# Performance work log

Measured on AMD Instinct MI355X. Metric: run time of the kernel, lower is better.

## Reference

```python
import math
import jax, jax.numpy as jnp
import numpy as np

D_MODEL = 768
N_HEAD = 12
N_BR = 4
DH = D_MODEL // N_HEAD          # 64
H_TOT = N_BR * N_HEAD           # 48
SCALE = math.pi / math.sqrt(3.0)
ATTNSCALE = DH ** -0.5


def _chebyshev(T, max_deg, dtype):
    # T_all[t, d] = Cheb poly T_d(x_t), x in [-1, 1]
    if T > 1:
        x = 2.0 * jnp.arange(T, dtype=dtype) / (T - 1) - 1.0
    else:
        x = jnp.zeros(1, dtype=dtype)
    cols = [jnp.ones_like(x), x]
    for _ in range(2, max_deg + 1):
        cols.append(2.0 * x * cols[-1] - cols[-2])
    return jnp.stack(cols, axis=1)  # (T, max_deg+1)


def setup_inputs() -> dict:
    key = jax.random.key(0)
    ks = jax.random.split(key, 12)
    s = 0.02
    return {
        "X": jax.random.normal(ks[0], (2, 1024, D_MODEL), jnp.float32),
        "Wq": jax.random.normal(ks[1], (D_MODEL * N_BR, D_MODEL), jnp.float32) * s,
        "bq": jax.random.normal(ks[2], (D_MODEL * N_BR,), jnp.float32) * s,
        "Wk": jax.random.normal(ks[3], (D_MODEL, D_MODEL), jnp.float32) * s,
        "bk": jax.random.normal(ks[4], (D_MODEL,), jnp.float32) * s,
        "Wv": jax.random.normal(ks[5], (D_MODEL, D_MODEL), jnp.float32) * s,
        "bv": jax.random.normal(ks[6], (D_MODEL,), jnp.float32) * s,
        "A": jax.random.normal(ks[7], (DH, DH), jnp.float32) * s,
        "id_bias": jax.random.normal(ks[8], (H_TOT, DH), jnp.float32) * s,
        "sink_scalars": jax.random.normal(ks[9], (H_TOT, 1, 1), jnp.float32) * s,
        "v_nulls": jax.random.normal(ks[10], (N_BR, D_MODEL), jnp.float32) * s,
        "Wo": jax.random.normal(ks[11], (N_BR, D_MODEL, D_MODEL), jnp.float32) * s,
        "bo": jnp.zeros((N_BR, D_MODEL), jnp.float32),
    }


def _attention(X, Wq, bq, Wk, bk, Wv, bv, A, id_bias, sink_scalars, v_nulls, Wo, bo):
    B, T, C = X.shape
    dtype = X.dtype

    # projections (torch Linear: x @ W.T + b)
    q = (X @ Wq.T + bq).reshape(B, T, H_TOT, DH).transpose(0, 2, 1, 3)   # (B,H_tot,T,Dh)
    v = (X @ Wv.T + bv).reshape(B, T, N_HEAD, DH).transpose(0, 2, 1, 3)
    v = jnp.tile(v, (1, N_BR, 1, 1))                                     # (B,H_tot,T,Dh)
    k = (X @ Wk.T + bk).reshape(B, T, N_HEAD, DH).transpose(0, 2, 1, 3)
    k = jnp.tile(k, (1, N_BR, 1, 1))

    # BiasedWedge on q
    S = (A - A.T)[None] + jax.vmap(jnp.diag)(id_bias)                    # (H_tot,Dh,Dh)
    q = q + jnp.einsum('bhtd,hde->bhte', q, S)

    # Chebyshev phase-vector rotation (custom RoPE)
    H = DH // 2
    max_deg = max(3, 2 * H)
    T_all = _chebyshev(T, max_deg, dtype)                                # (T, max_deg+1)
    frac = jnp.arange(H, dtype=dtype) / (H - 1) if H > 1 else jnp.zeros(1, dtype)
    n_f = jnp.clip(1 + jnp.round(frac * (max_deg - 2)).astype(jnp.int32), 1, max_deg - 1)
    raw1 = T_all[:, n_f]                                                 # (T,H)
    raw2 = T_all[:, n_f + 1]
    nrm = jnp.sqrt(raw1 * raw1 + raw2 * raw2 + 1e-8)
    base1 = (raw1 / nrm)[None, None]                                     # (1,1,T,H)
    base2 = (raw2 / nrm)[None, None]

    def apply_rot(x_in):
        x1, x2 = x_in[..., :H], x_in[..., H:]
        return jnp.concatenate([x1 * base1 - x2 * base2,
                                x1 * base2 + x2 * base1], axis=-1)

    q = apply_rot(q)
    k = apply_rot(k)

    # softplus-gated causal attention with learned sink
    scores = jnp.einsum('bhtd,bhsd->bhts', q, k) * ATTNSCALE             # (B,H_tot,T,T)
    key_self = jnp.maximum((k * k).sum(-1), 1e-6)                        # (B,H_tot,T)
    denom = jnp.sqrt(key_self)[:, :, None, :]
    w = jax.nn.softplus(scores / denom)
    causal = jnp.tril(jnp.ones((T, T), bool))                            # keep lower-tri
    w = jnp.where(causal, w, 0.0)
    w = w * jax.nn.sigmoid(SCALE * w)

    sinks = sink_scalars.reshape(1, H_TOT, 1, 1)                         # broadcast sink col
    alpha = 1.0 / (w.sum(-1, keepdims=True) + sinks + 1e-6)              # (B,H_tot,T,1)
    probs_tokens = w * alpha
    probs_sink = jnp.broadcast_to(sinks, (B, H_TOT, T, 1)) * alpha

    out_tokens = jnp.einsum('bhts,bhsd->bhtd', probs_tokens, v)
    v_null = v_nulls.reshape(H_TOT, DH)[None, :, None, :]                # (1,H_tot,1,Dh)
    context = out_tokens + probs_sink * v_null                           # (B,H_tot,T,Dh)

    context = context.reshape(B, N_BR, N_HEAD, T, DH)
    context = context.transpose(0, 1, 3, 2, 4).reshape(B, N_BR, T, C)
    y = jnp.einsum('bntc,ncd->bntd', context, Wo) + bo[None, :, None, :]
    return y.mean(axis=1)                                                # (B,T,C)


def reference(X, Wq, bq, Wk, bk, Wv, bv, A, id_bias, sink_scalars, v_nulls, Wo, bo):
    return _attention(X, Wq, bq, Wk, bk, Wv, bv, A, id_bias, sink_scalars, v_nulls, Wo, bo)
```

## Files before the change

kernel.cpp:

```cpp
#include <hip/hip_runtime.h>
#include <math.h>

#define B_ 2
#define T_ 1024
#define C_ 768
#define NH 12
#define NBR 4
#define DH_ 64
#define HT 48
#define MROWS (B_*T_)

#define SCALE_W 1.8137993642342178f
#define ATTNSCALE_ 0.125f

#define OFF_B1    0
#define OFF_B2    (OFF_B1 + 32768)
#define OFF_QKVB  (OFF_B2 + 32768)
#define OFF_BSUM  (OFF_QKVB + 4608)
#define OFF_WQKV  (OFF_BSUM + 768)
#define OFF_XB    (OFF_WQKV + 1769472)
#define OFF_WOT   (OFF_XB + 786432)
#define OFF_QF    (OFF_WOT + 1179648)
#define OFF_KF    (OFF_QF + 6291456)
#define OFF_VF    (OFF_KF + 1572864)
#define OFF_QB    OFF_KF
#define OFF_KB    (OFF_VF + 1572864)
#define OFF_VB    (OFF_KB + 786432)
#define OFF_RKS   (OFF_VB + 786432)
#define OFF_CTXB  OFF_QF

typedef __attribute__((ext_vector_type(8))) short short8t;
typedef __attribute__((ext_vector_type(4))) float f32x4;

__device__ inline ushort f2bf(float f) {
    union { float f; unsigned u; } v; v.f = f;
    unsigned r = (v.u + 0x7FFFu + ((v.u >> 16) & 1u)) >> 16;
    return (ushort)r;
}

typedef __attribute__((address_space(3))) void lds_vt;
typedef const __attribute__((address_space(1))) void gbl_vt;
static __device__ __forceinline__ void gload16(const void* g, void* l) {
    __builtin_amdgcn_global_load_lds((gbl_vt*)g, (lds_vt*)l, 16, 0, 0);
}

__global__ void cheb_kernel(float* __restrict__ ws) {
    int t = blockIdx.x * 256 + threadIdx.x;
    if (t >= T_) return;
    float* b1 = ws + OFF_B1 + t * 32;
    float* b2 = ws + OFF_B2 + t * 32;
    float x = 2.0f * (float)t / 1023.0f - 1.0f;
    float Tp = 1.0f, Tc = x;
    for (int j = 0; j < 32; j++) {
        float r1 = Tc;
        float r2 = 2.0f * x * Tc - Tp;
        float nr = sqrtf(r1 * r1 + r2 * r2 + 1e-8f);
        b1[j] = r1 / nr;
        b2[j] = r2 / nr;
        Tp = r2;
        Tc = 2.0f * x * r2 - r1;
    }
}

__global__ __launch_bounds__(256) void prep_wq(
    const float* __restrict__ Aw, const float* __restrict__ idb,
    const float* __restrict__ Wq, const float* __restrict__ bq,
    float* __restrict__ ws) {
    __shared__ float Ms[64][64];
    int h = blockIdx.x;
    int tid = threadIdx.x;
    for (int i = tid; i < 4096; i += 256) {
        int d = i >> 6, e = i & 63;
        float v = Aw[d * 64 + e] - Aw[e * 64 + d];
        if (d == e) v += 1.0f + idb[h * 64 + d];
        Ms[d][e] = v;
    }
    __syncthreads();
    int c = blockIdx.y * 256 + tid;
    float wq[64];
#pragma unroll
    for (int d = 0; d < 64; d++) wq[d] = Wq[(size_t)(h * 64 + d) * 768 + c];
    ushort* EWqb = (ushort*)(ws + OFF_WQKV);
    for (int e = 0; e < 64; e++) {
        float acc = 0.f;
#pragma unroll
        for (int d = 0; d < 64; d++) acc += Ms[d][e] * wq[d];
        EWqb[(size_t)(h * 64 + e) * 768 + c] = f2bf(acc);
    }
    if (blockIdx.y == 0 && tid < 64) {
        int e = tid;
        float acc = 0.f;
        for (int d = 0; d < 64; d++) acc += Ms[d][e] * bq[h * 64 + d];
        ws[OFF_QKVB + h * 64 + e] = acc;
    }
}

__global__ void conv_bf16(const float* __restrict__ src, ushort* __restrict__ dst) {
    int i = (blockIdx.x * 256 + threadIdx.x) * 4;
    float4 v = *(const float4*)(src + i);
    ushort4 o;
    o.x = f2bf(v.x); o.y = f2bf(v.y); o.z = f2bf(v.z); o.w = f2bf(v.w);
    *(ushort4*)(dst + i) = o;
}

__global__ __launch_bounds__(256) void woT_kernel(const float* __restrict__ Wo,
                                                  ushort* __restrict__ WoT) {
    __shared__ float tile[64][65];
    int nb = blockIdx.z;
    int k0 = blockIdx.x * 64, c0 = blockIdx.y * 64;
    int tx = threadIdx.x & 63, ty = threadIdx.x >> 6;
#pragma unroll
    for (int p = 0; p < 16; p++) {
        int ky = p * 4 + ty;
        tile[ky][tx] = Wo[((size_t)nb * 768 + k0 + ky) * 768 + c0 + tx];
    }
    __syncthreads();
#pragma unroll
    for (int p = 0; p < 16; p++) {
        int cy = p * 4 + ty;
        WoT[(size_t)(c0 + cy) * 3072 + nb * 768 + k0 + tx] = f2bf(tile[tx][cy]);
    }
}

__global__ void bias_prep(const float* __restrict__ bo, const float* __restrict__ bk,
                          const float* __restrict__ bv, float* __restrict__ ws) {
    int n = blockIdx.x * 256 + threadIdx.x;
    if (n < 768) {
        ws[OFF_BSUM + n] = 0.25f * (bo[n] + bo[768 + n] + bo[1536 + n] + bo[2304 + n]);
        ws[OFF_QKVB + 3072 + n] = bk[n];
        ws[OFF_QKVB + 3840 + n] = bv[n];
    }
}

__global__ void y_init(const float* __restrict__ bsum, float* __restrict__ Y) {
    int idx = (blockIdx.x * 256 + threadIdx.x) * 4;
    int n = idx - (idx / 768) * 768;
    float4 o = { bsum[n], bsum[n + 1], bsum[n + 2], bsum[n + 3] };
    *(float4*)(Y + idx) = o;
}

static __device__ __forceinline__ void gemm_kloop128(
    const ushort* __restrict__ A, const ushort* __restrict__ B, int K,
    int m0, int n0, int k_begin, int k_end,
    ushort* AsU, ushort* BsU, f32x4 acc[4][4], int tid) {
    char* As = (char*)AsU;
    char* Bs = (char*)BsU;
    int lane = tid & 63, w = tid >> 6;
    int g = lane >> 4, c = lane & 15;
    int wr = w >> 1, wc = w & 1;
    int srow[4], scol[4];
#pragma unroll
    for (int r = 0; r < 4; r++) {
        int p = r * 4096 + w * 1024 + lane * 16;
        int row = p >> 7;
        int bp = (p & 127) ^ ((row & 7) << 4);
        srow[r] = row;
        scol[r] = bp >> 1;
    }
    for (int k0 = k_begin; k0 < k_end; k0 += 64) {
        __syncthreads();
#pragma unroll
        for (int r = 0; r < 4; r++) {
            gload16(A + (size_t)(m0 + srow[r]) * K + k0 + scol[r],
                    As + r * 4096 + w * 1024);
            gload16(B + (size_t)(n0 + srow[r]) * K + k0 + scol[r],
                    Bs + r * 4096 + w * 1024);
        }
        __syncthreads();
#pragma unroll
        for (int kk = 0; kk < 2; kk++) {
            short8t af[4], bf[4];
#pragma unroll
            for (int i = 0; i < 4; i++) {
                int ra = wr * 64 + i * 16 + c;
                af[i] = *(const short8t*)(As + ra * 128 + ((kk * 64 + g * 16) ^ ((ra & 7) << 4)));
                int rb = wc * 64 + i * 16 + c;
                bf[i] = *(const short8t*)(Bs + rb * 128 + ((kk * 64 + g * 16) ^ ((rb & 7) << 4)));
            }
#pragma unroll
            for (int i = 0; i < 4; i++)
#pragma unroll
                for (int j = 0; j < 4; j++)
                    acc[i][j] = __builtin_amdgcn_mfma_f32_16x16x32_bf16(
                        af[i], bf[j], acc[i][j], 0, 0, 0);
        }
    }
}

__global__ __launch_bounds__(256) void gemm_qkv(
    const ushort* __restrict__ A, const ushort* __restrict__ Bw,
    const float* __restrict__ qkvbias,
    float* __restrict__ Q, float* __restrict__ Kf, float* __restrict__ Vf) {
    __shared__ __align__(16) ushort AsU[8192];
    __shared__ __align__(16) ushort BsU[8192];
    int tid = threadIdx.x;
    int lane = tid & 63, wid = tid >> 6;
    int wr = wid >> 1, wc = wid & 1;
    int g = lane >> 4, c = lane & 15;
    int m0 = blockIdx.x * 128, n0 = blockIdx.y * 128;
    f32x4 acc[4][4] = {};
    gemm_kloop128(A, Bw, 768, m0, n0, 0, 768, AsU, BsU, acc, tid);
    int y = blockIdx.y;
    float* outp; int nstr, nbase;
    if (y < 24)      { outp = Q;  nstr = 3072; nbase = 0; }
    else if (y < 30) { outp = Kf; nstr = 768;  nbase = 3072; }
    else             { outp = Vf; nstr = 768;  nbase = 3840; }
#pragma unroll
    for (int j = 0; j < 4; j++) {
        int n = n0 + wc * 64 + j * 16 + c;
        float bv = qkvbias[n];
#pragma unroll
        for (int i = 0; i < 4; i++) {
#pragma unroll
            for (int r = 0; r < 4; r++) {
                int m = m0 + wr * 64 + i * 16 + g * 4 + r;
                outp[(size_t)m * nstr + (n - nbase)] = acc[i][j][r] + bv;
            }
        }
    }
}

__global__ __launch_bounds__(256) void gemm_fin(
    const ushort* __restrict__ A, const ushort* __restrict__ Bw,
    float* __restrict__ Y) {
    __shared__ __align__(16) ushort AsU[8192];
    __shared__ __align__(16) ushort BsU[8192];
    int tid = threadIdx.x;
    int lane = tid & 63, wid = tid >> 6;
    int wr = wid >> 1, wc = wid & 1;
    int g = lane >> 4, c = lane & 15;
    int m0 = blockIdx.x * 128, n0 = blockIdx.y * 128;
    int kz = blockIdx.z * 1024;
    f32x4 acc[4][4] = {};
    gemm_kloop128(A, Bw, 3072, m0, n0, kz, kz + 1024, AsU, BsU, acc, tid);
#pragma unroll
    for (int j = 0; j < 4; j++) {
        int n = n0 + wc * 64 + j * 16 + c;
#pragma unroll
        for (int i = 0; i < 4; i++) {
#pragma unroll
            for (int r = 0; r < 4; r++) {
                int m = m0 + wr * 64 + i * 16 + g * 4 + r;
                atomicAdd(&Y[(size_t)m * 768 + n], 0.25f * acc[i][j][r]);
            }
        }
    }
}

__global__ void rot2_kernel(const float* __restrict__ in, int heads,
                            ushort* __restrict__ outb, float* __restrict__ rkso,
                            const float* __restrict__ ws) {
    int idx = blockIdx.x * 256 + threadIdx.x;
    if (idx >= MROWS * heads) return;
    int r = idx / heads;
    int hd = idx - r * heads;
    int tloc = r & (T_ - 1);
    int b = r >> 10;
    const float* p = in + (size_t)r * (heads * 64) + hd * 64;
    const float* b1 = ws + OFF_B1 + tloc * 32;
    const float* b2 = ws + OFF_B2 + tloc * 32;
    __align__(16) ushort ob[64];
    float nrm = 0.f;
#pragma unroll
    for (int i = 0; i < 8; i++) {
        float4 lo = *(const float4*)(p + i * 4);
        float4 hi = *(const float4*)(p + 32 + i * 4);
        float4 c1 = *(const float4*)(b1 + i * 4);
        float4 c2 = *(const float4*)(b2 + i * 4);
        float o1[4], o2[4];
        o1[0] = lo.x * c1.x - hi.x * c2.x;  o2[0] = lo.x * c2.x + hi.x * c1.x;
        o1[1] = lo.y * c1.y - hi.y * c2.y;  o2[1] = lo.y * c2.y + hi.y * c1.y;
        o1[2] = lo.z * c1.z - hi.z * c2.z;  o2[2] = lo.z * c2.z + hi.z * c1.z;
        o1[3] = lo.w * c1.w - hi.w * c2.w;  o2[3] = lo.w * c2.w + hi.w * c1.w;
#pragma unroll
        for (int j = 0; j < 4; j++) {
            ob[i * 4 + j]      = f2bf(o1[j]);
            ob[32 + i * 4 + j] = f2bf(o2[j]);
            nrm += o1[j] * o1[j] + o2[j] * o2[j];
        }
    }
    ushort* op = outb + ((size_t)(b * heads + hd) * T_ + tloc) * 64;
#pragma unroll
    for (int i = 0; i < 8; i++) *(int4*)(op + i * 8) = *(const int4*)&ob[i * 8];
    if (rkso) rkso[((b * heads + hd) << 10) + tloc] = ATTNSCALE_ / sqrtf(fmaxf(nrm, 1e-6f));
}

__global__ void vconv_kernel(const float* __restrict__ V, ushort* __restrict__ Vb) {
    int idx = blockIdx.x * 256 + threadIdx.x;
    int base = idx * 4;
    int row = base / 768, col = base - row * 768;
    int b = row >> 10, t = row & (T_ - 1);
    int hk = col >> 6, d = col & 63;
    float4 v = *(const float4*)(V + (size_t)row * 768 + col);
    ushort4 o;
    o.x = f2bf(v.x); o.y = f2bf(v.y); o.z = f2bf(v.z); o.w = f2bf(v.w);
    *(ushort4*)(Vb + ((size_t)((b * NH + hk) * T_ + t)) * 64 + d) = o;
}

__global__ __launch_bounds__(512) void attn_mfma2(
    const ushort* __restrict__ Qb, const ushort* __restrict__ Kb,
    const ushort* __restrict__ Vb, const float* __restrict__ rks,
    const float* __restrict__ sinks, const float* __restrict__ vnull,
    ushort* __restrict__ ctxb) {
    __shared__ __align__(16) ushort Ks[64][72];
    __shared__ __align__(16) ushort Vt[64][72];
    __shared__ __align__(16) ushort Ps[8][16][72];
    __shared__ float rk_s[64];
    int tid  = threadIdx.x;
    int lane = tid & 63;
    int wid  = tid >> 6;
    int p = 7 - blockIdx.x;
    int bh = blockIdx.y;
    int b = bh / HT, h = bh - b * HT;
    int hk = h % NH;
    int qt0 = p * 128;
    int g = lane >> 4;
    int c = lane & 15;
    int rowbase = qt0 + wid * 16;

    const ushort* qrow = Qb + ((size_t)(b * HT + h) * T_ + rowbase + c) * 64;
    short8t qa0 = *(const short8t*)(qrow + g * 8);
    short8t qa1 = *(const short8t*)(qrow + 32 + g * 8);

    f32x4 oacc[4] = {};
    float sumw[4] = {0.f, 0.f, 0.f, 0.f};

    const size_t kvbase = (size_t)(b * NH + hk) * T_;
    int nt = 2 * p + 2;
    int sr = tid >> 3;
    int sc = (tid & 7) * 8;
    for (int st = 0; st < nt; st++) {
        int s0 = st * 64;
        __syncthreads();
        {
            *(int4*)&Ks[sr][sc] = *(const int4*)(Kb + (kvbase + s0 + sr) * 64 + sc);
            __align__(16) ushort vv[8];
            *(int4*)&vv[0] = *(const int4*)(Vb + (kvbase + s0 + sr) * 64 + sc);
#pragma unroll
            for (int j = 0; j < 8; j++) Vt[sc + j][sr] = vv[j];
            if (tid < 64) rk_s[tid] = rks[kvbase + (size_t)s0 + tid];
        }
        __syncthreads();

        if (s0 > rowbase + 15) continue;

        f32x4 sfr[4];
#pragma unroll
        for (int f = 0; f < 4; f++) {
            f32x4 cacc = {0.f, 0.f, 0.f, 0.f};
            short8t kb0 = *(const short8t*)&Ks[f * 16 + c][g * 8];
            cacc = __builtin_amdgcn_mfma_f32_16x16x32_bf16(qa0, kb0, cacc, 0, 0, 0);
            short8t kb1 = *(const short8t*)&Ks[f * 16 + c][32 + g * 8];
            cacc = __builtin_amdgcn_mfma_f32_16x16x32_bf16(qa1, kb1, cacc, 0, 0, 0);
            sfr[f] = cacc;
        }

        bool diag = (s0 + 63 > rowbase);
#pragma unroll
        for (int f = 0; f < 4; f++) {
            int scol = f * 16 + c;
            float rkv = rk_s[scol];
#pragma unroll
            for (int r = 0; r < 4; r++) {
                int trow = g * 4 + r;
                float x = sfr[f][r] * rkv;
                float w = __logf(1.f + __expf(x));
                w = w * __builtin_amdgcn_rcpf(1.f + __expf(-SCALE_W * w));
                if (diag && s0 + scol > rowbase + trow) w = 0.f;
                sumw[r] += w;
                Ps[wid][trow][scol] = f2bf(w);
            }
        }

#pragma unroll
        for (int hf = 0; hf < 2; hf++) {
            short8t pa = *(const short8t*)&Ps[wid][c][hf * 32 + g * 8];
#pragma unroll
            for (int f = 0; f < 4; f++) {
                short8t vb = *(const short8t*)&Vt[f * 16 + c][hf * 32 + g * 8];
                oacc[f] = __builtin_amdgcn_mfma_f32_16x16x32_bf16(pa, vb, oacc[f], 0, 0, 0);
            }
        }
    }

#pragma unroll
    for (int m = 1; m < 16; m <<= 1) {
#pragma unroll
        for (int r = 0; r < 4; r++) sumw[r] += __shfl_xor(sumw[r], m, 64);
    }
    float skv = sinks[h];
    float alpha[4], ps[4];
#pragma unroll
    for (int r = 0; r < 4; r++) {
        alpha[r] = 1.0f / (sumw[r] + skv + 1e-6f);
        ps[r] = skv * alpha[r];
    }
    int nb = h / NH;
#pragma unroll
    for (int f = 0; f < 4; f++) {
        float vn = vnull[h * 64 + f * 16 + c];
#pragma unroll
        for (int r = 0; r < 4; r++) {
            int t = rowbase + g * 4 + r;
            ctxb[(size_t)(b * T_ + t) * 3072 + nb * 768 + hk * 64 + f * 16 + c]
                = f2bf(oacc[f][r] * alpha[r] + ps[r] * vn);
        }
    }
}

extern "C" void kernel_launch(void* const* d_in, const int* in_sizes, int n_in,
                              void* d_out, int out_size, void* d_ws, size_t ws_size,
                              hipStream_t stream) {
    const float* X   = (const float*)d_in[0];
    const float* Wq  = (const float*)d_in[1];
    const float* bq  = (const float*)d_in[2];
    const float* Wk  = (const float*)d_in[3];
    const float* bk  = (const float*)d_in[4];
    const float* Wv  = (const float*)d_in[5];
    const float* bv  = (const float*)d_in[6];
    const float* Aw  = (const float*)d_in[7];
    const float* idb = (const float*)d_in[8];
    const float* sk  = (const float*)d_in[9];
    const float* vn  = (const float*)d_in[10];
    const float* Wo  = (const float*)d_in[11];
    const float* bo  = (const float*)d_in[12];
    float* ws = (float*)d_ws;
    float* Y  = (float*)d_out;

    ushort* WQKV = (ushort*)(ws + OFF_WQKV);
    hipLaunchKernelGGL(cheb_kernel, dim3(4), dim3(256), 0, stream, ws);
    hipLaunchKernelGGL(prep_wq, dim3(48, 3), dim3(256), 0, stream, Aw, idb, Wq, bq, ws);
    hipLaunchKernelGGL(conv_bf16, dim3(576), dim3(256), 0, stream,
                       Wk, WQKV + (size_t)3072 * 768);
    hipLaunchKernelGGL(conv_bf16, dim3(576), dim3(256), 0, stream,
                       Wv, WQKV + (size_t)3840 * 768);
    hipLaunchKernelGGL(conv_bf16, dim3(1536), dim3(256), 0, stream,
                       X, (ushort*)(ws + OFF_XB));
    hipLaunchKernelGGL(woT_kernel, dim3(12, 12, 4), dim3(256), 0, stream,
                       Wo, (ushort*)(ws + OFF_WOT));
    hipLaunchKernelGGL(bias_prep, dim3(3), dim3(256), 0, stream, bo, bk, bv, ws);
    hipLaunchKernelGGL(gemm_qkv, dim3(16, 36), dim3(256), 0, stream,
                       (const ushort*)(ws + OFF_XB), WQKV, ws + OFF_QKVB,
                       ws + OFF_QF, ws + OFF_KF, ws + OFF_VF);
    hipLaunchKernelGGL(rot2_kernel, dim3(96), dim3(256), 0, stream,
                       ws + OFF_KF, NH, (ushort*)(ws + OFF_KB), ws + OFF_RKS, ws);
    hipLaunchKernelGGL(vconv_kernel, dim3(1536), dim3(256), 0, stream,
                       ws + OFF_VF, (ushort*)(ws + OFF_VB));
    hipLaunchKernelGGL(rot2_kernel, dim3(384), dim3(256), 0, stream,
                       ws + OFF_QF, HT, (ushort*)(ws + OFF_QB), (float*)nullptr, ws);
    hipLaunchKernelGGL(attn_mfma2, dim3(8, 96), dim3(512), 0, stream,
                       (const ushort*)(ws + OFF_QB), (const ushort*)(ws + OFF_KB),
                       (const ushort*)(ws + OFF_VB), ws + OFF_RKS, sk, vn,
                       (ushort*)(ws + OFF_CTXB));
    hipLaunchKernelGGL(y_init, dim3(1536), dim3(256), 0, stream, ws + OFF_BSUM, Y);
    hipLaunchKernelGGL(gemm_fin, dim3(16, 6, 3), dim3(256), 0, stream,
                       (const ushort*)(ws + OFF_CTXB), (const ushort*)(ws + OFF_WOT), Y);
}
```

Baseline: 328.4 us.

## Share K/V tiles across four branch heads and pre-transpose V with swizzled LDS

The attention kernel now runs one block per (batch, KV head) and loops over the four branch query heads inside, so each K/V tile is loaded into shared memory once instead of four times. V is transposed to a d-major bf16 layout by a new LDS-tiled conversion kernel, which removes the per-element scatter transpose in the attention loop. K and V tiles are loaded with direct global-to-LDS loads (gload16) into XOR-swizzled layouts to avoid bank conflicts. The grid shrinks from 768 to 192 blocks and each thread holds four times the accumulators, which raises register pressure and may hurt occupancy and load balance.

Measured after the change: 363.8 us. +10.8%, slower.

```diff
diff --git a/kernel.cpp b/kernel.cpp
--- a/kernel.cpp
+++ b/kernel.cpp
@@ -285,125 +285,149 @@
     if (rkso) rkso[((b * heads + hd) << 10) + tloc] = ATTNSCALE_ / sqrtf(fmaxf(nrm, 1e-6f));
 }
 
-__global__ void vconv_kernel(const float* __restrict__ V, ushort* __restrict__ Vb) {
-    int idx = blockIdx.x * 256 + threadIdx.x;
-    int base = idx * 4;
-    int row = base / 768, col = base - row * 768;
-    int b = row >> 10, t = row & (T_ - 1);
-    int hk = col >> 6, d = col & 63;
-    float4 v = *(const float4*)(V + (size_t)row * 768 + col);
-    ushort4 o;
-    o.x = f2bf(v.x); o.y = f2bf(v.y); o.z = f2bf(v.z); o.w = f2bf(v.w);
-    *(ushort4*)(Vb + ((size_t)((b * NH + hk) * T_ + t)) * 64 + d) = o;
-}
-
-__global__ __launch_bounds__(512) void attn_mfma2(
+__global__ __launch_bounds__(256) void vconvT_kernel(const float* __restrict__ V,
+                                                     ushort* __restrict__ VbT) {
+    __shared__ float tile[64][65];
+    int head = blockIdx.y;
+    int b = head / NH, hk = head - b * NH;
+    int t0 = blockIdx.x * 64;
+    int tx = threadIdx.x & 63, ty = threadIdx.x >> 6;
+#pragma unroll
+    for (int p = 0; p < 16; p++) {
+        int trow = p * 4 + ty;
+        tile[trow][tx] = V[(size_t)(b * T_ + t0 + trow) * 768 + hk * 64 + tx];
+    }
+    __syncthreads();
+#pragma unroll
+    for (int p = 0; p < 16; p++) {
+        int d = p * 4 + ty;
+        VbT[(size_t)head * 65536 + (size_t)d * 1024 + t0 + tx] = f2bf(tile[tx][d]);
+    }
+}
+
+__global__ __launch_bounds__(512) void attn_mfma3(
     const ushort* __restrict__ Qb, const ushort* __restrict__ Kb,
-    const ushort* __restrict__ Vb, const float* __restrict__ rks,
+    const ushort* __restrict__ VbT, const float* __restrict__ rks,
     const float* __restrict__ sinks, const float* __restrict__ vnull,
     ushort* __restrict__ ctxb) {
-    __shared__ __align__(16) ushort Ks[64][72];
-    __shared__ __align__(16) ushort Vt[64][72];
-    __shared__ __align__(16) ushort Ps[8][16][72];
+    __shared__ __align__(16) char KsB[8192];
+    __shared__ __align__(16) char VtB[8192];
+    __shared__ __align__(16) char PsB[8][2048];
     __shared__ float rk_s[64];
     int tid  = threadIdx.x;
     int lane = tid & 63;
     int wid  = tid >> 6;
-    int p = 7 - blockIdx.x;
+    int p  = 7 - blockIdx.x;
     int bh = blockIdx.y;
-    int b = bh / HT, h = bh - b * HT;
-    int hk = h % NH;
+    int b = bh / NH, hk = bh - b * NH;
     int qt0 = p * 128;
     int g = lane >> 4;
     int c = lane & 15;
     int rowbase = qt0 + wid * 16;
 
-    const ushort* qrow = Qb + ((size_t)(b * HT + h) * T_ + rowbase + c) * 64;
-    short8t qa0 = *(const short8t*)(qrow + g * 8);
-    short8t qa1 = *(const short8t*)(qrow + 32 + g * 8);
-
-    f32x4 oacc[4] = {};
-    float sumw[4] = {0.f, 0.f, 0.f, 0.f};
+    short8t qa0[4], qa1[4];
+#pragma unroll
+    for (int nb = 0; nb < 4; nb++) {
+        const ushort* qrow = Qb +
+            ((size_t)(b * HT + nb * NH + hk) * T_ + rowbase + c) * 64;
+        qa0[nb] = *(const short8t*)(qrow + g * 8);
+        qa1[nb] = *(const short8t*)(qrow + 32 + g * 8);
+    }
+
+    f32x4 oacc[4][4] = {};
+    float sumw[4][4] = {};
 
     const size_t kvbase = (size_t)(b * NH + hk) * T_;
+    const ushort* Kt0 = Kb + kvbase * 64;
+    const ushort* Vt0 = VbT + kvbase * 64;
+    int drow  = tid >> 3;
+    int sbyte = ((tid & 7) * 16) ^ ((drow & 7) << 4);
+    int scolu = sbyte >> 1;
+    char* ldsK = KsB + wid * 1024;
+    char* ldsV = VtB + wid * 1024;
+
     int nt = 2 * p + 2;
-    int sr = tid >> 3;
-    int sc = (tid & 7) * 8;
     for (int st = 0; st < nt; st++) {
         int s0 = st * 64;
         __syncthreads();
-        {
-            *(int4*)&Ks[sr][sc] = *(const int4*)(Kb + (kvbase + s0 + sr) * 64 + sc);
-            __align__(16) ushort vv[8];
-            *(int4*)&vv[0] = *(const int4*)(Vb + (kvbase + s0 + sr) * 64 + sc);
-#pragma unroll
-            for (int j = 0; j < 8; j++) Vt[sc + j][sr] = vv[j];
-            if (tid < 64) rk_s[tid] = rks[kvbase + (size_t)s0 + tid];
-        }
+        gload16(Kt0 + (size_t)(s0 + drow) * 64 + scolu, ldsK);
+        gload16(Vt0 + (size_t)drow * 1024 + s0 + scolu, ldsV);
+        if (tid < 64) rk_s[tid] = rks[kvbase + (size_t)s0 + tid];
         __syncthreads();
 
         if (s0 > rowbase + 15) continue;
-
-        f32x4 sfr[4];
+        bool diag = (s0 + 63 > rowbase);
+        char* Ps = PsB[wid];
+
+#pragma unroll
+        for (int nb = 0; nb < 4; nb++) {
+            f32x4 sfr[4];
+#pragma unroll
+            for (int f = 0; f < 4; f++) {
+                int row = f * 16 + c, sw = (row & 7) << 4;
+                f32x4 cacc = {0.f, 0.f, 0.f, 0.f};
+                short8t kb0 = *(const short8t*)(KsB + row * 128 + ((g * 16) ^ sw));
+                cacc = __builtin_amdgcn_mfma_f32_16x16x32_bf16(qa0[nb], kb0, cacc, 0, 0, 0);
+                short8t kb1 = *(const short8t*)(KsB + row * 128 + ((64 + g * 16) ^ sw));
+                cacc = __builtin_amdgcn_mfma_f32_16x16x32_bf16(qa1[nb], kb1, cacc, 0, 0, 0);
+                sfr[f] = cacc;
+            }
+#pragma unroll
+            for (int f = 0; f < 4; f++) {
+                int scol = f * 16 + c;
+                float rkv = rk_s[scol];
+#pragma unroll
+                for (int r = 0; r < 4; r++) {
+                    int trow = g * 4 + r;
+                    float x = sfr[f][r] * rkv;
+                    float w = __logf(1.f + __expf(x));
+                    w = w * __builtin_amdgcn_rcpf(1.f + __expf(-SCALE_W * w));
+                    if (diag && s0 + scol > rowbase + trow) w = 0.f;
+                    sumw[nb][r] += w;
+                    *(ushort*)(Ps + trow * 128 + ((scol * 2) ^ ((trow & 7) << 4))) = f2bf(w);
+                }
+            }
+#pragma unroll
+            for (int hf = 0; hf < 2; hf++) {
+                short8t pa = *(const short8t*)(Ps + c * 128 +
+                                               ((hf * 64 + g * 16) ^ ((c & 7) << 4)));
+#pragma unroll
+                for (int f = 0; f < 4; f++) {
+                    int row = f * 16 + c;
+                    short8t vb = *(const short8t*)(VtB + row * 128 +
+                                                   ((hf * 64 + g * 16) ^ ((row & 7) << 4)));
+                    oacc[nb][f] = __builtin_amdgcn_mfma_f32_16x16x32_bf16(
+                        pa, vb, oacc[nb][f], 0, 0, 0);
+                }
+            }
+        }
+    }
+
+#pragma unroll
+    for (int nb = 0; nb < 4; nb++) {
+#pragma unroll
+        for (int m = 1; m < 16; m <<= 1) {
+#pragma unroll
+            for (int r = 0; r < 4; r++)
+                sumw[nb][r] += __shfl_xor(sumw[nb][r], m, 64);
+        }
+        int h = nb * NH + hk;
+        float skv = sinks[h];
+        float alpha[4], ps[4];
+#pragma unroll
+        for (int r = 0; r < 4; r++) {
+            alpha[r] = 1.0f / (sumw[nb][r] + skv + 1e-6f);
+            ps[r] = skv * alpha[r];
+        }
 #pragma unroll
         for (int f = 0; f < 4; f++) {
-            f32x4 cacc = {0.f, 0.f, 0.f, 0.f};
-            short8t kb0 = *(const short8t*)&Ks[f * 16 + c][g * 8];
-            cacc = __builtin_amdgcn_mfma_f32_16x16x32_bf16(qa0, kb0, cacc, 0, 0, 0);
-            short8t kb1 = *(const short8t*)&Ks[f * 16 + c][32 + g * 8];
-            cacc = __builtin_amdgcn_mfma_f32_16x16x32_bf16(qa1, kb1, cacc, 0, 0, 0);
-            sfr[f] = cacc;
-        }
-
-        bool diag = (s0 + 63 > rowbase);
-#pragma unroll
-        for (int f = 0; f < 4; f++) {
-            int scol = f * 16 + c;
-            float rkv = rk_s[scol];
+            float vnv = vnull[h * 64 + f * 16 + c];
 #pragma unroll
             for (int r = 0; r < 4; r++) {
-                int trow = g * 4 + r;
-                float x = sfr[f][r] * rkv;
-                float w = __logf(1.f + __expf(x));
-                w = w * __builtin_amdgcn_rcpf(1.f + __expf(-SCALE_W * w));
-                if (diag && s0 + scol > rowbase + trow) w = 0.f;
-                sumw[r] += w;
-                Ps[wid][trow][scol] = f2bf(w);
-            }
-        }
-
-#pragma unroll
-        for (int hf = 0; hf < 2; hf++) {
-            short8t pa = *(const short8t*)&Ps[wid][c][hf * 32 + g * 8];
-#pragma unroll
-            for (int f = 0; f < 4; f++) {
-                short8t vb = *(const short8t*)&Vt[f * 16 + c][hf * 32 + g * 8];
-                oacc[f] = __builtin_amdgcn_mfma_f32_16x16x32_bf16(pa, vb, oacc[f], 0, 0, 0);
-            }
-        }
-    }
-
-#pragma unroll
-    for (int m = 1; m < 16; m <<= 1) {
-#pragma unroll
-        for (int r = 0; r < 4; r++) sumw[r] += __shfl_xor(sumw[r], m, 64);
-    }
-    float skv = sinks[h];
-    float alpha[4], ps[4];
-#pragma unroll
-    for (int r = 0; r < 4; r++) {
-        alpha[r] = 1.0f / (sumw[r] + skv + 1e-6f);
-        ps[r] = skv * alpha[r];
-    }
-    int nb = h / NH;
-#pragma unroll
-    for (int f = 0; f < 4; f++) {
-        float vn = vnull[h * 64 + f * 16 + c];
-#pragma unroll
-        for (int r = 0; r < 4; r++) {
-            int t = rowbase + g * 4 + r;
-            ctxb[(size_t)(b * T_ + t) * 3072 + nb * 768 + hk * 64 + f * 16 + c]
-                = f2bf(oacc[f][r] * alpha[r] + ps[r] * vn);
+                int t = rowbase + g * 4 + r;
+                ctxb[(size_t)(b * T_ + t) * 3072 + nb * 768 + hk * 64 + f * 16 + c]
+                    = f2bf(oacc[nb][f][r] * alpha[r] + ps[r] * vnv);
+            }
         }
     }
 }
@@ -444,11 +468,11 @@
                        ws + OFF_QF, ws + OFF_KF, ws + OFF_VF);
     hipLaunchKernelGGL(rot2_kernel, dim3(96), dim3(256), 0, stream,
                        ws + OFF_KF, NH, (ushort*)(ws + OFF_KB), ws + OFF_RKS, ws);
-    hipLaunchKernelGGL(vconv_kernel, dim3(1536), dim3(256), 0, stream,
+    hipLaunchKernelGGL(vconvT_kernel, dim3(16, 24), dim3(256), 0, stream,
                        ws + OFF_VF, (ushort*)(ws + OFF_VB));
     hipLaunchKernelGGL(rot2_kernel, dim3(384), dim3(256), 0, stream,
                        ws + OFF_QF, HT, (ushort*)(ws + OFF_QB), (float*)nullptr, ws);
-    hipLaunchKernelGGL(attn_mfma2, dim3(8, 96), dim3(512), 0, stream,
+    hipLaunchKernelGGL(attn_mfma3, dim3(8, 24), dim3(512), 0, stream,
                        (const ushort*)(ws + OFF_QB), (const ushort*)(ws + OFF_KB),
                        (const ushort*)(ws + OFF_VB), ws + OFF_RKS, sk, vn,
                        (ushort*)(ws + OFF_CTXB));
```
